# Performance work log

Measured on AMD Instinct MI355X. Metric: run time of the kernel, lower is better.

## Reference

```python
import jax, jax.numpy as jnp
import numpy as np

B, N, D, H, C = 16, 196, 768, 3072, 10

def setup_inputs() -> dict:
    key = jax.random.key(0)
    ks = jax.random.split(key, 8)
    s1 = 1.0 / np.sqrt(D)
    s2 = 1.0 / np.sqrt(H)
    return {
        "x": jax.random.normal(ks[0], (B, N, D), jnp.float32),
        "y": jax.random.randint(ks[1], (B,), 0, C),
        "W1": jax.random.normal(ks[2], (H, D), jnp.float32) * s1,
        "b1": jax.random.normal(ks[3], (H,), jnp.float32) * 0.01,
        "W2": jax.random.normal(ks[4], (D, H), jnp.float32) * s2,
        "b2": jax.random.normal(ks[5], (D,), jnp.float32) * 0.01,
        "mask_fc1": jax.random.uniform(ks[6], (C, H, D), jnp.float32),
        "mask_fc2": jax.random.uniform(ks[7], (C, D, H), jnp.float32),
    }

def reference(x, y, W1, b1, W2, b2, mask_fc1, mask_fc2):
    # per-sample masked weights: [B, out, in]
    Wm1 = W1[None, :, :] * mask_fc1[y]          # [B, H, D]
    h = jnp.einsum('bni,boi->bno', x, Wm1) + b1  # [B, N, H]
    h = jax.nn.gelu(h, approximate=False)        # act (drop1/norm are identity)
    Wm2 = W2[None, :, :] * mask_fc2[y]           # [B, D, H]
    out = jnp.einsum('bni,boi->bno', h, Wm2) + b2  # [B, N, D]
    return out
```

## Files before the change

### kernel.cpp

```cpp
#include <hip/hip_runtime.h>
#include <hip/hip_bf16.h>
#include <math.h>

#define B_ 16
#define N_ 196
#define D_ 768
#define H_ 3072
#define C_ 10
#define MPAD 256

typedef __attribute__((ext_vector_type(8))) short bf16x8;
typedef __attribute__((ext_vector_type(4))) float f32x4;

__device__ __forceinline__ ushort f2bu(float f) {
    union { float f; unsigned u; } c; c.f = f;
    unsigned u = c.u;
    unsigned r = (u + 0x7FFFu + ((u >> 16) & 1u)) >> 16;
    return (ushort)r;
}

__device__ __forceinline__ void gl_lds16(const ushort* g, ushort* l) {
    __builtin_amdgcn_global_load_lds(
        (const __attribute__((address_space(1))) void*)g,
        (__attribute__((address_space(3))) void*)l, 16, 0, 0);
}

__device__ __forceinline__ void build_wm_chunk(
    const float* __restrict__ W, const float* __restrict__ mask,
    const int* __restrict__ y, ushort* __restrict__ outw,
    int c, int chunk)
{
    bool used = false;
    #pragma unroll
    for (int t = 0; t < B_; ++t) used |= (y[t] == c);
    if (!used) return;
    const long n = (long)H_ * D_;
    const long i = (long)chunk * 2048 + threadIdx.x * 8;
    const float4* wp = reinterpret_cast<const float4*>(W + i);
    const float4* mp = reinterpret_cast<const float4*>(mask + c * n + i);
    float4 w0 = wp[0], w1 = wp[1], m0 = mp[0], m1 = mp[1];
    ushort t8[8] = { f2bu(w0.x*m0.x), f2bu(w0.y*m0.y), f2bu(w0.z*m0.z), f2bu(w0.w*m0.w),
                     f2bu(w1.x*m1.x), f2bu(w1.y*m1.y), f2bu(w1.z*m1.z), f2bu(w1.w*m1.w) };
    *reinterpret_cast<uint4*>(outw + c * n + i) = *reinterpret_cast<const uint4*>(t8);
}

template<int EPI>
__device__ __forceinline__ void gemm_core(
    const ushort* __restrict__ A0, const ushort* __restrict__ Wm,
    const int* __restrict__ y, const float* __restrict__ bias1,
    ushort* __restrict__ hout, float* __restrict__ pout,
    int ot, int mt, int b, int sk)
{
    constexpr int K = (EPI == 0) ? D_ : H_;
    __shared__ ushort As[128][64];
    __shared__ ushort Bs[128][64];

    const int cls = y[b];
    const int tid = threadIdx.x, lane = tid & 63, wid = tid >> 6;
    const int wm = wid >> 1, wn = wid & 1;
    const int fr = lane & 15, fq = lane >> 4;
    const int lr = lane >> 3, le = (lane & 7) * 8;

    const ushort* Ab = A0 + ((long)b * MPAD + mt * 128) * K;
    const ushort* Bb = Wm + (long)cls * ((long)H_ * D_) + (long)(ot * 128) * K;

    f32x4 acc[4][4] = {};
    const int kt0 = (EPI == 0) ? 0 : sk * 12;

    #pragma unroll
    for (int t = 0; t < 12; ++t) {
        const int k0 = (kt0 + t) * 64;
        #pragma unroll
        for (int i = 0; i < 4; ++i) {
            const int r = wid * 32 + i * 8;
            gl_lds16(Ab + (long)(r + lr) * K + k0 + le, &As[r][0]);
        }
        #pragma unroll
        for (int i = 0; i < 4; ++i) {
            const int r = wid * 32 + i * 8;
            gl_lds16(Bb + (long)(r + lr) * K + k0 + le, &Bs[r][0]);
        }
        __syncthreads();
        #pragma unroll
        for (int kk = 0; kk < 64; kk += 32) {
            bf16x8 af[4], bf[4];
            #pragma unroll
            for (int i = 0; i < 4; ++i)
                af[i] = *reinterpret_cast<const bf16x8*>(&As[wm*64 + i*16 + fr][kk + fq*8]);
            #pragma unroll
            for (int j = 0; j < 4; ++j)
                bf[j] = *reinterpret_cast<const bf16x8*>(&Bs[wn*64 + j*16 + fr][kk + fq*8]);
            #pragma unroll
            for (int i = 0; i < 4; ++i)
                #pragma unroll
                for (int j = 0; j < 4; ++j)
                    acc[i][j] = __builtin_amdgcn_mfma_f32_16x16x32_bf16(af[i], bf[j], acc[i][j], 0, 0, 0);
        }
        __syncthreads();
    }

    if (EPI == 0) {
        #pragma unroll
        for (int j = 0; j < 4; ++j) {
            const int o = ot*128 + wn*64 + j*16 + fr;
            const float bias = bias1[o];
            #pragma unroll
            for (int i = 0; i < 4; ++i) {
                #pragma unroll
                for (int e = 0; e < 4; ++e) {
                    const int m = mt*128 + wm*64 + i*16 + fq*4 + e;
                    float v = acc[i][j][e] + bias;
                    v = 0.5f * v * (1.0f + erff(v * 0.70710678118654752f));
                    hout[((long)b * MPAD + m) * H_ + o] = f2bu(v);
                }
            }
        }
    } else {
        float* op = pout + (size_t)sk * (size_t)(B_ * N_ * D_);
        #pragma unroll
        for (int j = 0; j < 4; ++j) {
            const int o = ot*128 + wn*64 + j*16 + fr;
            #pragma unroll
            for (int i = 0; i < 4; ++i) {
                #pragma unroll
                for (int e = 0; e < 4; ++e) {
                    const int m = mt*128 + wm*64 + i*16 + fq*4 + e;
                    if (m < N_)
                        op[((long)b * N_ + m) * D_ + o] = acc[i][j][e];
                }
            }
        }
    }
}

__global__ __launch_bounds__(256) void prep1(
    const float* __restrict__ x, const int* __restrict__ y,
    const float* __restrict__ W1, const float* __restrict__ mask1,
    ushort* __restrict__ xb, ushort* __restrict__ wm1)
{
    const int bid = blockIdx.x;
    if (bid < 11520) {
        build_wm_chunk(W1, mask1, y, wm1, bid / 1152, bid % 1152);
    } else {
        const int i = (bid - 11520) * 256 + threadIdx.x;
        const int r = i / 96;
        const int c8 = (i % 96) * 8;
        const int b = r / 196, n = r - b * 196;
        const float4* src = reinterpret_cast<const float4*>(x + (long)r * D_ + c8);
        float4 a = src[0], bb = src[1];
        ushort t[8] = { f2bu(a.x), f2bu(a.y), f2bu(a.z), f2bu(a.w),
                        f2bu(bb.x), f2bu(bb.y), f2bu(bb.z), f2bu(bb.w) };
        *reinterpret_cast<uint4*>(xb + ((long)b * MPAD + n) * D_ + c8) =
            *reinterpret_cast<const uint4*>(t);
    }
}

__global__ __launch_bounds__(256) void fat2(
    const ushort* __restrict__ xb, const ushort* __restrict__ wm1,
    const int* __restrict__ y, const float* __restrict__ b1,
    ushort* __restrict__ h,
    const float* __restrict__ W2, const float* __restrict__ mask2,
    ushort* __restrict__ wm2)
{
    const int bid = blockIdx.x;
    if (bid < 768) {
        const int ot = bid % 24, mt = (bid / 24) & 1, b = bid / 48;
        gemm_core<0>(xb, wm1, y, b1, h, nullptr, ot, mt, b, 0);
    } else {
        const int idx = bid - 768;
        build_wm_chunk(W2, mask2, y, wm2, idx / 1152, idx % 1152);
    }
}

__global__ __launch_bounds__(256) void mgemm2(
    const ushort* __restrict__ h, const ushort* __restrict__ wm2,
    const int* __restrict__ y, float* __restrict__ part)
{
    const int ot = blockIdx.x, mt = blockIdx.y, z = blockIdx.z;
    gemm_core<1>(h, wm2, y, nullptr, nullptr, part, ot, mt, z >> 2, z & 3);
}

__global__ __launch_bounds__(256) void reduce_k(const float* __restrict__ part,
                                                const float* __restrict__ b2,
                                                float* __restrict__ out, int SK)
{
    const int i = blockIdx.x * 256 + threadIdx.x;
    const int stride4 = B_ * N_ * D_ / 4;
    float4 s = reinterpret_cast<const float4*>(part)[i];
    for (int k = 1; k < SK; ++k) {
        float4 p = reinterpret_cast<const float4*>(part)[(size_t)k * stride4 + i];
        s.x += p.x; s.y += p.y; s.z += p.z; s.w += p.w;
    }
    const int ob = (i % (D_ / 4)) * 4;
    float4 bias = *reinterpret_cast<const float4*>(b2 + ob);
    s.x += bias.x; s.y += bias.y; s.z += bias.z; s.w += bias.w;
    reinterpret_cast<float4*>(out)[i] = s;
}

__global__ __launch_bounds__(256) void fb_gemm1(
    const float* __restrict__ x, const int* __restrict__ y,
    const float* __restrict__ W1, const float* __restrict__ b1,
    const float* __restrict__ mask1, ushort* __restrict__ h)
{
    __shared__ ushort As[128][72];
    __shared__ ushort Bs[64][72];
    const int ot = blockIdx.x, mt = blockIdx.y, b = blockIdx.z;
    const int cls = y[b];
    const int tid = threadIdx.x, lane = tid & 63, wid = tid >> 6;
    const int wm = wid >> 1, wn = wid & 1;
    const int fr = lane & 15, fq = lane >> 4;
    const int sr = tid >> 2, sc = (tid & 3) * 16;
    f32x4 acc[4][2] = {};
    const long xbase = ((long)b * N_) * D_;
    const long wbase = (long)(ot * 64) * D_;
    const long mbase = ((long)cls * H_ + ot * 64) * D_;
    for (int kt = 0; kt < D_ / 64; ++kt) {
        const int k0 = kt * 64 + sc;
        #pragma unroll
        for (int half = 0; half < 2; ++half) {
            const int r = sr + half * 64;
            const int m = mt * 128 + r;
            ushort tmp[16];
            if (m < N_) {
                const float4* src = reinterpret_cast<const float4*>(x + xbase + (long)m * D_ + k0);
                #pragma unroll
                for (int j = 0; j < 4; ++j) {
                    float4 v = src[j];
                    tmp[4*j+0]=f2bu(v.x); tmp[4*j+1]=f2bu(v.y); tmp[4*j+2]=f2bu(v.z); tmp[4*j+3]=f2bu(v.w);
                }
            } else { for (int j = 0; j < 16; ++j) tmp[j] = 0; }
            *reinterpret_cast<uint4*>(&As[r][sc])   = *reinterpret_cast<const uint4*>(&tmp[0]);
            *reinterpret_cast<uint4*>(&As[r][sc+8]) = *reinterpret_cast<const uint4*>(&tmp[8]);
        }
        {
            const float4* wsrc = reinterpret_cast<const float4*>(W1 + wbase + (long)sr * D_ + k0);
            const float4* msrc = reinterpret_cast<const float4*>(mask1 + mbase + (long)sr * D_ + k0);
            ushort tmp[16];
            #pragma unroll
            for (int j = 0; j < 4; ++j) {
                float4 wv = wsrc[j], mv = msrc[j];
                tmp[4*j+0]=f2bu(wv.x*mv.x); tmp[4*j+1]=f2bu(wv.y*mv.y);
                tmp[4*j+2]=f2bu(wv.z*mv.z); tmp[4*j+3]=f2bu(wv.w*mv.w);
            }
            *reinterpret_cast<uint4*>(&Bs[sr][sc])   = *reinterpret_cast<const uint4*>(&tmp[0]);
            *reinterpret_cast<uint4*>(&Bs[sr][sc+8]) = *reinterpret_cast<const uint4*>(&tmp[8]);
        }
        __syncthreads();
        #pragma unroll
        for (int kk = 0; kk < 64; kk += 32) {
            bf16x8 af[4], bf[2];
            #pragma unroll
            for (int i = 0; i < 4; ++i) af[i] = *reinterpret_cast<const bf16x8*>(&As[wm*64+i*16+fr][kk+fq*8]);
            #pragma unroll
            for (int j = 0; j < 2; ++j) bf[j] = *reinterpret_cast<const bf16x8*>(&Bs[wn*32+j*16+fr][kk+fq*8]);
            #pragma unroll
            for (int i = 0; i < 4; ++i)
                #pragma unroll
                for (int j = 0; j < 2; ++j)
                    acc[i][j] = __builtin_amdgcn_mfma_f32_16x16x32_bf16(af[i], bf[j], acc[i][j], 0, 0, 0);
        }
        __syncthreads();
    }
    #pragma unroll
    for (int j = 0; j < 2; ++j) {
        const int o = ot*64 + wn*32 + j*16 + fr;
        const float bias = b1[o];
        #pragma unroll
        for (int i = 0; i < 4; ++i)
            #pragma unroll
            for (int e = 0; e < 4; ++e) {
                const int m = mt*128 + wm*64 + i*16 + fq*4 + e;
                if (m < N_) {
                    float v = acc[i][j][e] + bias;
                    v = 0.5f * v * (1.0f + erff(v * 0.70710678118654752f));
                    h[(((long)b * N_) + m) * H_ + o] = f2bu(v);
                }
            }
    }
}

__global__ __launch_bounds__(256) void fb_gemm2(
    const ushort* __restrict__ h, const int* __restrict__ y,
    const float* __restrict__ W2, const float* __restrict__ b2,
    const float* __restrict__ mask2, float* __restrict__ dst,
    int split, int nkt, int add_bias)
{
    __shared__ ushort As[128][72];
    __shared__ ushort Bs[64][72];
    const int ot = blockIdx.x, mt = blockIdx.y, z = blockIdx.z;
    const int b = z / split, sk = z - b * split;
    const int cls = y[b];
    const int tid = threadIdx.x, lane = tid & 63, wid = tid >> 6;
    const int wm = wid >> 1, wn = wid & 1;
    const int fr = lane & 15, fq = lane >> 4;
    const int sr = tid >> 2, sc = (tid & 3) * 16;
    f32x4 acc[4][2] = {};
    const long hbase = ((long)b * N_) * H_;
    const long wbase = (long)(ot * 64) * H_;
    const long mbase = ((long)cls * D_ + ot * 64) * H_;
    const int kt0 = sk * nkt;
    for (int kt = kt0; kt < kt0 + nkt; ++kt) {
        const int k0 = kt * 64 + sc;
        #pragma unroll
        for (int half = 0; half < 2; ++half) {
            const int r = sr + half * 64;
            const int m = mt * 128 + r;
            if (m < N_) {
                const uint4* src = reinterpret_cast<const uint4*>(h + hbase + (long)m * H_ + k0);
                *reinterpret_cast<uint4*>(&As[r][sc])   = src[0];
                *reinterpret_cast<uint4*>(&As[r][sc+8]) = src[1];
            } else {
                uint4 z4 = {0u,0u,0u,0u};
                *reinterpret_cast<uint4*>(&As[r][sc])   = z4;
                *reinterpret_cast<uint4*>(&As[r][sc+8]) = z4;
            }
        }
        {
            const float4* wsrc = reinterpret_cast<const float4*>(W2 + wbase + (long)sr * H_ + k0);
            const float4* msrc = reinterpret_cast<const float4*>(mask2 + mbase + (long)sr * H_ + k0);
            ushort tmp[16];
            #pragma unroll
            for (int j = 0; j < 4; ++j) {
                float4 wv = wsrc[j], mv = msrc[j];
                tmp[4*j+0]=f2bu(wv.x*mv.x); tmp[4*j+1]=f2bu(wv.y*mv.y);
                tmp[4*j+2]=f2bu(wv.z*mv.z); tmp[4*j+3]=f2bu(wv.w*mv.w);
            }
            *reinterpret_cast<uint4*>(&Bs[sr][sc])   = *reinterpret_cast<const uint4*>(&tmp[0]);
            *reinterpret_cast<uint4*>(&Bs[sr][sc+8]) = *reinterpret_cast<const uint4*>(&tmp[8]);
        }
        __syncthreads();
        #pragma unroll
        for (int kk = 0; kk < 64; kk += 32) {
            bf16x8 af[4], bf[2];
            #pragma unroll
            for (int i = 0; i < 4; ++i) af[i] = *reinterpret_cast<const bf16x8*>(&As[wm*64+i*16+fr][kk+fq*8]);
            #pragma unroll
            for (int j = 0; j < 2; ++j) bf[j] = *reinterpret_cast<const bf16x8*>(&Bs[wn*32+j*16+fr][kk+fq*8]);
            #pragma unroll
            for (int i = 0; i < 4; ++i)
                #pragma unroll
                for (int j = 0; j < 2; ++j)
                    acc[i][j] = __builtin_amdgcn_mfma_f32_16x16x32_bf16(af[i], bf[j], acc[i][j], 0, 0, 0);
        }
        __syncthreads();
    }
    float* op = dst + (size_t)sk * (size_t)(B_ * N_ * D_);
    #pragma unroll
    for (int j = 0; j < 2; ++j) {
        const int o = ot*64 + wn*32 + j*16 + fr;
        const float bias = add_bias ? b2[o] : 0.0f;
        #pragma unroll
        for (int i = 0; i < 4; ++i)
            #pragma unroll
            for (int e = 0; e < 4; ++e) {
                const int m = mt*128 + wm*64 + i*16 + fq*4 + e;
                if (m < N_) op[(((long)b * N_) + m) * D_ + o] = acc[i][j][e] + bias;
            }
    }
}

extern "C" void kernel_launch(void* const* d_in, const int* in_sizes, int n_in,
                              void* d_out, int out_size, void* d_ws, size_t ws_size,
                              hipStream_t stream) {
    const float* x  = (const float*)d_in[0];
    const int*   y  = (const int*)d_in[1];
    const float* W1 = (const float*)d_in[2];
    const float* b1 = (const float*)d_in[3];
    const float* W2 = (const float*)d_in[4];
    const float* b2 = (const float*)d_in[5];
    const float* m1 = (const float*)d_in[6];
    const float* m2 = (const float*)d_in[7];
    float* out = (float*)d_out;

    const size_t xbB  = (size_t)B_ * MPAD * D_ * 2;
    const size_t hB   = (size_t)B_ * MPAD * H_ * 2;
    const size_t oB   = (size_t)B_ * N_ * D_ * 4;
    const size_t wmB  = (size_t)C_ * H_ * D_ * 2;

    const size_t off_xb   = 0;
    const size_t off_h    = off_xb + xbB;
    const size_t off_part = off_h + hB;
    const size_t off_wm1  = off_part + 4 * oB;
    const size_t off_wm2  = off_wm1 + wmB;
    const size_t need     = off_wm2 + wmB;

    if (ws_size >= need) {
        ushort* xb  = (ushort*)((char*)d_ws + off_xb);
        ushort* h   = (ushort*)((char*)d_ws + off_h);
        float* part = (float*)((char*)d_ws + off_part);
        ushort* wm1 = (ushort*)((char*)d_ws + off_wm1);
        ushort* wm2 = (ushort*)((char*)d_ws + off_wm2);

        prep1<<<11520 + 1176, 256, 0, stream>>>(x, y, W1, m1, xb, wm1);
        fat2<<<768 + 11520, 256, 0, stream>>>(xb, wm1, y, b1, h, W2, m2, wm2);
        mgemm2<<<dim3(6, 2, 64), 256, 0, stream>>>(h, wm2, y, part);
        reduce_k<<<(B_ * N_ * D_ / 4) / 256, 256, 0, stream>>>(part, b2, out, 4);
    } else {
        const size_t fb_hB = (size_t)B_ * N_ * H_ * 2;
        ushort* h = (ushort*)d_ws;
        int SK = 0;
        if      (ws_size >= fb_hB + 4 * oB) SK = 4;
        else if (ws_size >= fb_hB + 2 * oB) SK = 2;
        float* part = (float*)((char*)d_ws + fb_hB);
        dim3 g1(H_ / 64, 2, B_);
        fb_gemm1<<<g1, 256, 0, stream>>>(x, y, W1, b1, m1, h);
        if (SK) {
            dim3 g2(D_ / 64, 2, B_ * SK);
            fb_gemm2<<<g2, 256, 0, stream>>>(h, y, W2, b2, m2, part, SK, 48 / SK, 0);
            reduce_k<<<(B_ * N_ * D_ / 4) / 256, 256, 0, stream>>>(part, b2, out, SK);
        } else {
            dim3 g2(D_ / 64, 2, B_);
            fb_gemm2<<<g2, 256, 0, stream>>>(h, y, W2, b2, m2, out, 1, 48, 1);
        }
    }
}
```

Before: 142.1 us.

## Merge weight-mask prep into one grid-stride kernel and halve GEMM N-tiles

All masked-weight builds for both layers and the x conversion now run in a single persistent grid-stride prep kernel, and the used-class set is computed once as a bitmask. The layer-2 weight build is no longer co-scheduled with GEMM1. Both GEMMs move from 128x128 to 128x64 output tiles, doubling the block count (1536 blocks each) for better CU fill on the many-CU device. The cost is more A-tile reloads per output and lower MFMA work per LDS load.

```diff
diff --git a/kernel.cpp b/kernel.cpp
--- a/kernel.cpp
+++ b/kernel.cpp
@@ -19,156 +19,130 @@
     return (ushort)r;
 }
 
+__device__ __forceinline__ uint2 pack4(float4 a, float4 b) {
+    ushort t[4] = { f2bu(a.x*b.x), f2bu(a.y*b.y), f2bu(a.z*b.z), f2bu(a.w*b.w) };
+    return *reinterpret_cast<const uint2*>(t);
+}
+
 __device__ __forceinline__ void gl_lds16(const ushort* g, ushort* l) {
     __builtin_amdgcn_global_load_lds(
         (const __attribute__((address_space(1))) void*)g,
         (__attribute__((address_space(3))) void*)l, 16, 0, 0);
 }
 
-__device__ __forceinline__ void build_wm_chunk(
-    const float* __restrict__ W, const float* __restrict__ mask,
-    const int* __restrict__ y, ushort* __restrict__ outw,
-    int c, int chunk)
-{
-    bool used = false;
-    #pragma unroll
-    for (int t = 0; t < B_; ++t) used |= (y[t] == c);
-    if (!used) return;
-    const long n = (long)H_ * D_;
-    const long i = (long)chunk * 2048 + threadIdx.x * 8;
-    const float4* wp = reinterpret_cast<const float4*>(W + i);
-    const float4* mp = reinterpret_cast<const float4*>(mask + c * n + i);
-    float4 w0 = wp[0], w1 = wp[1], m0 = mp[0], m1 = mp[1];
-    ushort t8[8] = { f2bu(w0.x*m0.x), f2bu(w0.y*m0.y), f2bu(w0.z*m0.z), f2bu(w0.w*m0.w),
-                     f2bu(w1.x*m1.x), f2bu(w1.y*m1.y), f2bu(w1.z*m1.z), f2bu(w1.w*m1.w) };
-    *reinterpret_cast<uint4*>(outw + c * n + i) = *reinterpret_cast<const uint4*>(t8);
-}
-
-template<int EPI>
-__device__ __forceinline__ void gemm_core(
-    const ushort* __restrict__ A0, const ushort* __restrict__ Wm,
-    const int* __restrict__ y, const float* __restrict__ bias1,
-    ushort* __restrict__ hout, float* __restrict__ pout,
-    int ot, int mt, int b, int sk)
-{
-    constexpr int K = (EPI == 0) ? D_ : H_;
+__global__ __launch_bounds__(256) void prep_all(
+    const float* __restrict__ x, const int* __restrict__ y,
+    const float* __restrict__ W1, const float* __restrict__ m1,
+    const float* __restrict__ W2, const float* __restrict__ m2,
+    ushort* __restrict__ xb, ushort* __restrict__ wm1, ushort* __restrict__ wm2)
+{
+    unsigned used = 0;
+    #pragma unroll
+    for (int t = 0; t < B_; ++t) used |= (1u << y[t]);
+    const int tid = threadIdx.x;
+
+    for (int u = blockIdx.x; u < 12108; u += gridDim.x) {
+        if (u < 11520) {
+            const int layer = u / 5760;
+            const int v = u - layer * 5760;
+            const int c = v / 576, chunk = v - (v / 576) * 576;
+            if (!((used >> c) & 1)) continue;
+            const float* W = layer ? W2 : W1;
+            const float* M = layer ? m2 : m1;
+            ushort*     O = layer ? wm2 : wm1;
+            const long n = (long)H_ * D_;
+            const float4* wp = reinterpret_cast<const float4*>(W + (long)chunk * 4096);
+            const float4* mp = reinterpret_cast<const float4*>(M + c * n + (long)chunk * 4096);
+            float4 w0 = wp[tid], w1 = wp[tid+256], w2v = wp[tid+512], w3 = wp[tid+768];
+            float4 q0 = mp[tid], q1 = mp[tid+256], q2  = mp[tid+512], q3 = mp[tid+768];
+            uint2* op = reinterpret_cast<uint2*>(O + c * n + (long)chunk * 4096);
+            op[tid]     = pack4(w0, q0);
+            op[tid+256] = pack4(w1, q1);
+            op[tid+512] = pack4(w2v, q2);
+            op[tid+768] = pack4(w3, q3);
+        } else {
+            const int v = u - 11520;
+            const float4* xp = reinterpret_cast<const float4*>(x);
+            const float4 one = {1.f, 1.f, 1.f, 1.f};
+            #pragma unroll
+            for (int k = 0; k < 4; ++k) {
+                const int i4 = v * 1024 + tid + k * 256;
+                const int r  = i4 / 192;
+                const int c4 = i4 - r * 192;
+                const int b = r / N_, nn = r - b * N_;
+                float4 a = xp[i4];
+                *reinterpret_cast<uint2*>(xb + ((long)b * MPAD + nn) * D_ + c4 * 4) =
+                    pack4(a, one);
+            }
+        }
+    }
+}
+
+__global__ __launch_bounds__(256) void mgemm1(
+    const ushort* __restrict__ xb, const ushort* __restrict__ wm1,
+    const int* __restrict__ y, const float* __restrict__ b1,
+    ushort* __restrict__ h)
+{
     __shared__ ushort As[128][64];
-    __shared__ ushort Bs[128][64];
-
+    __shared__ ushort Bs[64][64];
+    const int ot = blockIdx.x;
+    const int mt = blockIdx.y;
+    const int b  = blockIdx.z;
     const int cls = y[b];
     const int tid = threadIdx.x, lane = tid & 63, wid = tid >> 6;
     const int wm = wid >> 1, wn = wid & 1;
     const int fr = lane & 15, fq = lane >> 4;
     const int lr = lane >> 3, le = (lane & 7) * 8;
 
-    const ushort* Ab = A0 + ((long)b * MPAD + mt * 128) * K;
-    const ushort* Bb = Wm + (long)cls * ((long)H_ * D_) + (long)(ot * 128) * K;
-
-    f32x4 acc[4][4] = {};
-    const int kt0 = (EPI == 0) ? 0 : sk * 12;
-
+    const ushort* Ab = xb + ((long)b * MPAD + mt * 128) * D_;
+    const ushort* Bb = wm1 + (long)cls * ((long)H_ * D_) + (long)(ot * 64) * D_;
+
+    f32x4 acc[4][2] = {};
     #pragma unroll
     for (int t = 0; t < 12; ++t) {
-        const int k0 = (kt0 + t) * 64;
+        const int k0 = t * 64;
         #pragma unroll
         for (int i = 0; i < 4; ++i) {
             const int r = wid * 32 + i * 8;
-            gl_lds16(Ab + (long)(r + lr) * K + k0 + le, &As[r][0]);
-        }
+            gl_lds16(Ab + (long)(r + lr) * D_ + k0 + le, &As[r][0]);
+        }
+        #pragma unroll
+        for (int i = 0; i < 2; ++i) {
+            const int r = wid * 16 + i * 8;
+            gl_lds16(Bb + (long)(r + lr) * D_ + k0 + le, &Bs[r][0]);
+        }
+        __syncthreads();
+        #pragma unroll
+        for (int kk = 0; kk < 64; kk += 32) {
+            bf16x8 af[4], bf[2];
+            #pragma unroll
+            for (int i = 0; i < 4; ++i)
+                af[i] = *reinterpret_cast<const bf16x8*>(&As[wm*64 + i*16 + fr][kk + fq*8]);
+            #pragma unroll
+            for (int j = 0; j < 2; ++j)
+                bf[j] = *reinterpret_cast<const bf16x8*>(&Bs[wn*32 + j*16 + fr][kk + fq*8]);
+            #pragma unroll
+            for (int i = 0; i < 4; ++i)
+                #pragma unroll
+                for (int j = 0; j < 2; ++j)
+                    acc[i][j] = __builtin_amdgcn_mfma_f32_16x16x32_bf16(af[i], bf[j], acc[i][j], 0, 0, 0);
+        }
+        __syncthreads();
+    }
+    #pragma unroll
+    for (int j = 0; j < 2; ++j) {
+        const int o = ot*64 + wn*32 + j*16 + fr;
+        const float bias = b1[o];
         #pragma unroll
         for (int i = 0; i < 4; ++i) {
-            const int r = wid * 32 + i * 8;
-            gl_lds16(Bb + (long)(r + lr) * K + k0 + le, &Bs[r][0]);
-        }
-        __syncthreads();
-        #pragma unroll
-        for (int kk = 0; kk < 64; kk += 32) {
-            bf16x8 af[4], bf[4];
-            #pragma unroll
-            for (int i = 0; i < 4; ++i)
-                af[i] = *reinterpret_cast<const bf16x8*>(&As[wm*64 + i*16 + fr][kk + fq*8]);
-            #pragma unroll
-            for (int j = 0; j < 4; ++j)
-                bf[j] = *reinterpret_cast<const bf16x8*>(&Bs[wn*64 + j*16 + fr][kk + fq*8]);
-            #pragma unroll
-            for (int i = 0; i < 4; ++i)
-                #pragma unroll
-                for (int j = 0; j < 4; ++j)
-                    acc[i][j] = __builtin_amdgcn_mfma_f32_16x16x32_bf16(af[i], bf[j], acc[i][j], 0, 0, 0);
-        }
-        __syncthreads();
-    }
-
-    if (EPI == 0) {
-        #pragma unroll
-        for (int j = 0; j < 4; ++j) {
-            const int o = ot*128 + wn*64 + j*16 + fr;
-            const float bias = bias1[o];
-            #pragma unroll
-            for (int i = 0; i < 4; ++i) {
-                #pragma unroll
-                for (int e = 0; e < 4; ++e) {
-                    const int m = mt*128 + wm*64 + i*16 + fq*4 + e;
-                    float v = acc[i][j][e] + bias;
-                    v = 0.5f * v * (1.0f + erff(v * 0.70710678118654752f));
-                    hout[((long)b * MPAD + m) * H_ + o] = f2bu(v);
-                }
-            }
-        }
-    } else {
-        float* op = pout + (size_t)sk * (size_t)(B_ * N_ * D_);
-        #pragma unroll
-        for (int j = 0; j < 4; ++j) {
-            const int o = ot*128 + wn*64 + j*16 + fr;
-            #pragma unroll
-            for (int i = 0; i < 4; ++i) {
-                #pragma unroll
-                for (int e = 0; e < 4; ++e) {
-                    const int m = mt*128 + wm*64 + i*16 + fq*4 + e;
-                    if (m < N_)
-                        op[((long)b * N_ + m) * D_ + o] = acc[i][j][e];
-                }
-            }
-        }
-    }
-}
-
-__global__ __launch_bounds__(256) void prep1(
-    const float* __restrict__ x, const int* __restrict__ y,
-    const float* __restrict__ W1, const float* __restrict__ mask1,
-    ushort* __restrict__ xb, ushort* __restrict__ wm1)
-{
-    const int bid = blockIdx.x;
-    if (bid < 11520) {
-        build_wm_chunk(W1, mask1, y, wm1, bid / 1152, bid % 1152);
-    } else {
-        const int i = (bid - 11520) * 256 + threadIdx.x;
-        const int r = i / 96;
-        const int c8 = (i % 96) * 8;
-        const int b = r / 196, n = r - b * 196;
-        const float4* src = reinterpret_cast<const float4*>(x + (long)r * D_ + c8);
-        float4 a = src[0], bb = src[1];
-        ushort t[8] = { f2bu(a.x), f2bu(a.y), f2bu(a.z), f2bu(a.w),
-                        f2bu(bb.x), f2bu(bb.y), f2bu(bb.z), f2bu(bb.w) };
-        *reinterpret_cast<uint4*>(xb + ((long)b * MPAD + n) * D_ + c8) =
-            *reinterpret_cast<const uint4*>(t);
-    }
-}
-
-__global__ __launch_bounds__(256) void fat2(
-    const ushort* __restrict__ xb, const ushort* __restrict__ wm1,
-    const int* __restrict__ y, const float* __restrict__ b1,
-    ushort* __restrict__ h,
-    const float* __restrict__ W2, const float* __restrict__ mask2,
-    ushort* __restrict__ wm2)
-{
-    const int bid = blockIdx.x;
-    if (bid < 768) {
-        const int ot = bid % 24, mt = (bid / 24) & 1, b = bid / 48;
-        gemm_core<0>(xb, wm1, y, b1, h, nullptr, ot, mt, b, 0);
-    } else {
-        const int idx = bid - 768;
-        build_wm_chunk(W2, mask2, y, wm2, idx / 1152, idx % 1152);
+            #pragma unroll
+            for (int e = 0; e < 4; ++e) {
+                const int m = mt*128 + wm*64 + i*16 + fq*4 + e;
+                float v = acc[i][j][e] + bias;
+                v = 0.5f * v * (1.0f + erff(v * 0.70710678118654752f));
+                h[((long)b * MPAD + m) * H_ + o] = f2bu(v);
+            }
+        }
     }
 }
 
@@ -176,8 +150,68 @@
     const ushort* __restrict__ h, const ushort* __restrict__ wm2,
     const int* __restrict__ y, float* __restrict__ part)
 {
-    const int ot = blockIdx.x, mt = blockIdx.y, z = blockIdx.z;
-    gemm_core<1>(h, wm2, y, nullptr, nullptr, part, ot, mt, z >> 2, z & 3);
+    __shared__ ushort As[128][64];
+    __shared__ ushort Bs[64][64];
+    const int ot = blockIdx.x;
+    const int mt = blockIdx.y;
+    const int z  = blockIdx.z;
+    const int b = z >> 2, sk = z & 3;
+    const int cls = y[b];
+    const int tid = threadIdx.x, lane = tid & 63, wid = tid >> 6;
+    const int wm = wid >> 1, wn = wid & 1;
+    const int fr = lane & 15, fq = lane >> 4;
+    const int lr = lane >> 3, le = (lane & 7) * 8;
+
+    const ushort* Ab = h + ((long)b * MPAD + mt * 128) * H_;
+    const ushort* Bb = wm2 + (long)cls * ((long)H_ * D_) + (long)(ot * 64) * H_;
+
+    f32x4 acc[4][2] = {};
+    const int kt0 = sk * 12;
+    #pragma unroll
+    for (int t = 0; t < 12; ++t) {
+        const int k0 = (kt0 + t) * 64;
+        #pragma unroll
+        for (int i = 0; i < 4; ++i) {
+            const int r = wid * 32 + i * 8;
+            gl_lds16(Ab + (long)(r + lr) * H_ + k0 + le, &As[r][0]);
+        }
+        #pragma unroll
+        for (int i = 0; i < 2; ++i) {
+            const int r = wid * 16 + i * 8;
+            gl_lds16(Bb + (long)(r + lr) * H_ + k0 + le, &Bs[r][0]);
+        }
+        __syncthreads();
+        #pragma unroll
+        for (int kk = 0; kk < 64; kk += 32) {
+            bf16x8 af[4], bf[2];
+            #pragma unroll
+            for (int i = 0; i < 4; ++i)
+                af[i] = *reinterpret_cast<const bf16x8*>(&As[wm*64 + i*16 + fr][kk + fq*8]);
+            #pragma unroll
+            for (int j = 0; j < 2; ++j)
+                bf[j] = *reinterpret_cast<const bf16x8*>(&Bs[wn*32 + j*16 + fr][kk + fq*8]);
+            #pragma unroll
+            for (int i = 0; i < 4; ++i)
+                #pragma unroll
+                for (int j = 0; j < 2; ++j)
+                    acc[i][j] = __builtin_amdgcn_mfma_f32_16x16x32_bf16(af[i], bf[j], acc[i][j], 0, 0, 0);
+        }
+        __syncthreads();
+    }
+    float* op = part + (size_t)sk * (size_t)(B_ * N_ * D_);
+    #pragma unroll
+    for (int j = 0; j < 2; ++j) {
+        const int o = ot*64 + wn*32 + j*16 + fr;
+        #pragma unroll
+        for (int i = 0; i < 4; ++i) {
+            #pragma unroll
+            for (int e = 0; e < 4; ++e) {
+                const int m = mt*128 + wm*64 + i*16 + fq*4 + e;
+                if (m < N_)
+                    op[((long)b * N_ + m) * D_ + o] = acc[i][j][e];
+            }
+        }
+    }
 }
 
 __global__ __launch_bounds__(256) void reduce_k(const float* __restrict__ part,
@@ -391,9 +425,9 @@
         ushort* wm1 = (ushort*)((char*)d_ws + off_wm1);
         ushort* wm2 = (ushort*)((char*)d_ws + off_wm2);
 
-        prep1<<<11520 + 1176, 256, 0, stream>>>(x, y, W1, m1, xb, wm1);
-        fat2<<<768 + 11520, 256, 0, stream>>>(xb, wm1, y, b1, h, W2, m2, wm2);
-        mgemm2<<<dim3(6, 2, 64), 256, 0, stream>>>(h, wm2, y, part);
+        prep_all<<<2048, 256, 0, stream>>>(x, y, W1, m1, W2, m2, xb, wm1, wm2);
+        mgemm1<<<dim3(48, 2, 16), 256, 0, stream>>>(xb, wm1, y, b1, h);
+        mgemm2<<<dim3(12, 2, 64), 256, 0, stream>>>(h, wm2, y, part);
         reduce_k<<<(B_ * N_ * D_ / 4) / 256, 256, 0, stream>>>(part, b2, out, 4);
     } else {
         const size_t fb_hB = (size_t)B_ * N_ * H_ * 2;
```

Result: slower. 161.6 us (+13.8%).

## Double-buffer GEMM LDS tiles, halve N-tile, and merge weight prep into one kernel

Applied to the files above, without the earlier changes.

Both masked-weight builds (fc1 and fc2) and the x conversion now run in a single prep kernel. This removes the fused GEMM1-plus-W2-prep kernel, and GEMM1 becomes a plain launch. The GEMM core now double-buffers the A and B tiles in LDS, issuing the next tile's global-to-LDS loads before the current tile's MFMAs, so memory latency overlaps compute. It also shrinks the output tile from 128 to 64 columns, which doubles the grid and improves occupancy and CU coverage. The trade-offs are more A-tile reloads per output and the loss of the earlier overlap between GEMM1 and W2 preparation.

```diff
diff --git a/kernel.cpp b/kernel.cpp
--- a/kernel.cpp
+++ b/kernel.cpp
@@ -25,23 +25,45 @@
         (__attribute__((address_space(3))) void*)l, 16, 0, 0);
 }
 
-__device__ __forceinline__ void build_wm_chunk(
-    const float* __restrict__ W, const float* __restrict__ mask,
-    const int* __restrict__ y, ushort* __restrict__ outw,
-    int c, int chunk)
-{
-    bool used = false;
-    #pragma unroll
-    for (int t = 0; t < B_; ++t) used |= (y[t] == c);
-    if (!used) return;
-    const long n = (long)H_ * D_;
-    const long i = (long)chunk * 2048 + threadIdx.x * 8;
-    const float4* wp = reinterpret_cast<const float4*>(W + i);
-    const float4* mp = reinterpret_cast<const float4*>(mask + c * n + i);
-    float4 w0 = wp[0], w1 = wp[1], m0 = mp[0], m1 = mp[1];
-    ushort t8[8] = { f2bu(w0.x*m0.x), f2bu(w0.y*m0.y), f2bu(w0.z*m0.z), f2bu(w0.w*m0.w),
-                     f2bu(w1.x*m1.x), f2bu(w1.y*m1.y), f2bu(w1.z*m1.z), f2bu(w1.w*m1.w) };
-    *reinterpret_cast<uint4*>(outw + c * n + i) = *reinterpret_cast<const uint4*>(t8);
+__global__ __launch_bounds__(256) void prep_all(
+    const float* __restrict__ x, const int* __restrict__ y,
+    const float* __restrict__ W1, const float* __restrict__ m1,
+    const float* __restrict__ W2, const float* __restrict__ m2,
+    ushort* __restrict__ xb, ushort* __restrict__ wm1, ushort* __restrict__ wm2)
+{
+    const int bid = blockIdx.x;
+    const int tid = threadIdx.x;
+    if (bid < 23040) {
+        const int layer = bid / 11520;
+        const int v = bid - layer * 11520;
+        const int c = v / 1152, chunk = v - c * 1152;
+        bool used = false;
+        #pragma unroll
+        for (int t = 0; t < B_; ++t) used |= (y[t] == c);
+        if (!used) return;
+        const float* W = layer ? W2 : W1;
+        const float* M = layer ? m2 : m1;
+        ushort*      O = layer ? wm2 : wm1;
+        const long n = (long)H_ * D_;
+        const long i = (long)chunk * 2048 + tid * 8;
+        const float4* wp = reinterpret_cast<const float4*>(W + i);
+        const float4* mp = reinterpret_cast<const float4*>(M + c * n + i);
+        float4 w0 = wp[0], w1 = wp[1], q0 = mp[0], q1 = mp[1];
+        ushort t8[8] = { f2bu(w0.x*q0.x), f2bu(w0.y*q0.y), f2bu(w0.z*q0.z), f2bu(w0.w*q0.w),
+                         f2bu(w1.x*q1.x), f2bu(w1.y*q1.y), f2bu(w1.z*q1.z), f2bu(w1.w*q1.w) };
+        *reinterpret_cast<uint4*>(O + c * n + i) = *reinterpret_cast<const uint4*>(t8);
+    } else {
+        const int i = (bid - 23040) * 256 + tid;
+        const int r = i / 96;
+        const int c8 = (i % 96) * 8;
+        const int b = r / N_, nn = r - b * N_;
+        const float4* src = reinterpret_cast<const float4*>(x + (long)r * D_ + c8);
+        float4 a = src[0], bb = src[1];
+        ushort t8[8] = { f2bu(a.x), f2bu(a.y), f2bu(a.z), f2bu(a.w),
+                         f2bu(bb.x), f2bu(bb.y), f2bu(bb.z), f2bu(bb.w) };
+        *reinterpret_cast<uint4*>(xb + ((long)b * MPAD + nn) * D_ + c8) =
+            *reinterpret_cast<const uint4*>(t8);
+    }
 }
 
 template<int EPI>
@@ -52,8 +74,9 @@
     int ot, int mt, int b, int sk)
 {
     constexpr int K = (EPI == 0) ? D_ : H_;
-    __shared__ ushort As[128][64];
-    __shared__ ushort Bs[128][64];
+    constexpr int NT = 12;
+    __shared__ ushort As[2][128][64];
+    __shared__ ushort Bs[2][64][64];
 
     const int cls = y[b];
     const int tid = threadIdx.x, lane = tid & 63, wid = tid >> 6;
@@ -62,47 +85,67 @@
     const int lr = lane >> 3, le = (lane & 7) * 8;
 
     const ushort* Ab = A0 + ((long)b * MPAD + mt * 128) * K;
-    const ushort* Bb = Wm + (long)cls * ((long)H_ * D_) + (long)(ot * 128) * K;
-
-    f32x4 acc[4][4] = {};
-    const int kt0 = (EPI == 0) ? 0 : sk * 12;
-
-    #pragma unroll
-    for (int t = 0; t < 12; ++t) {
-        const int k0 = (kt0 + t) * 64;
+    const ushort* Bb = Wm + (long)cls * ((long)H_ * D_) + (long)(ot * 64) * K;
+    const int kt0 = (EPI == 0) ? 0 : sk * NT;
+
+    {
+        const int k0 = kt0 * 64;
         #pragma unroll
         for (int i = 0; i < 4; ++i) {
             const int r = wid * 32 + i * 8;
-            gl_lds16(Ab + (long)(r + lr) * K + k0 + le, &As[r][0]);
-        }
-        #pragma unroll
-        for (int i = 0; i < 4; ++i) {
-            const int r = wid * 32 + i * 8;
-            gl_lds16(Bb + (long)(r + lr) * K + k0 + le, &Bs[r][0]);
-        }
-        __syncthreads();
+            gl_lds16(Ab + (long)(r + lr) * K + k0 + le, &As[0][r][0]);
+        }
+        #pragma unroll
+        for (int i = 0; i < 2; ++i) {
+            const int r = wid * 16 + i * 8;
+            gl_lds16(Bb + (long)(r + lr) * K + k0 + le, &Bs[0][r][0]);
+        }
+    }
+    asm volatile("s_waitcnt vmcnt(0)" ::: "memory");
+    __builtin_amdgcn_sched_barrier(0);
+    __builtin_amdgcn_s_barrier();
+
+    f32x4 acc[4][2] = {};
+    #pragma unroll
+    for (int t = 0; t < NT; ++t) {
+        const int cur = t & 1;
+        if (t + 1 < NT) {
+            const int k0 = (kt0 + t + 1) * 64;
+            #pragma unroll
+            for (int i = 0; i < 4; ++i) {
+                const int r = wid * 32 + i * 8;
+                gl_lds16(Ab + (long)(r + lr) * K + k0 + le, &As[cur ^ 1][r][0]);
+            }
+            #pragma unroll
+            for (int i = 0; i < 2; ++i) {
+                const int r = wid * 16 + i * 8;
+                gl_lds16(Bb + (long)(r + lr) * K + k0 + le, &Bs[cur ^ 1][r][0]);
+            }
+        }
         #pragma unroll
         for (int kk = 0; kk < 64; kk += 32) {
-            bf16x8 af[4], bf[4];
+            bf16x8 af[4], bf[2];
             #pragma unroll
             for (int i = 0; i < 4; ++i)
-                af[i] = *reinterpret_cast<const bf16x8*>(&As[wm*64 + i*16 + fr][kk + fq*8]);
-            #pragma unroll
-            for (int j = 0; j < 4; ++j)
-                bf[j] = *reinterpret_cast<const bf16x8*>(&Bs[wn*64 + j*16 + fr][kk + fq*8]);
+                af[i] = *reinterpret_cast<const bf16x8*>(&As[cur][wm*64 + i*16 + fr][kk + fq*8]);
+            #pragma unroll
+            for (int j = 0; j < 2; ++j)
+                bf[j] = *reinterpret_cast<const bf16x8*>(&Bs[cur][wn*32 + j*16 + fr][kk + fq*8]);
             #pragma unroll
             for (int i = 0; i < 4; ++i)
                 #pragma unroll
-                for (int j = 0; j < 4; ++j)
+                for (int j = 0; j < 2; ++j)
                     acc[i][j] = __builtin_amdgcn_mfma_f32_16x16x32_bf16(af[i], bf[j], acc[i][j], 0, 0, 0);
         }
-        __syncthreads();
+        asm volatile("s_waitcnt vmcnt(0)" ::: "memory");
+        __builtin_amdgcn_sched_barrier(0);
+        __builtin_amdgcn_s_barrier();
     }
 
     if (EPI == 0) {
         #pragma unroll
-        for (int j = 0; j < 4; ++j) {
-            const int o = ot*128 + wn*64 + j*16 + fr;
+        for (int j = 0; j < 2; ++j) {
+            const int o = ot*64 + wn*32 + j*16 + fr;
             const float bias = bias1[o];
             #pragma unroll
             for (int i = 0; i < 4; ++i) {
@@ -118,8 +161,8 @@
     } else {
         float* op = pout + (size_t)sk * (size_t)(B_ * N_ * D_);
         #pragma unroll
-        for (int j = 0; j < 4; ++j) {
-            const int o = ot*128 + wn*64 + j*16 + fr;
+        for (int j = 0; j < 2; ++j) {
+            const int o = ot*64 + wn*32 + j*16 + fr;
             #pragma unroll
             for (int i = 0; i < 4; ++i) {
                 #pragma unroll
@@ -133,51 +176,20 @@
     }
 }
 
-__global__ __launch_bounds__(256) void prep1(
-    const float* __restrict__ x, const int* __restrict__ y,
-    const float* __restrict__ W1, const float* __restrict__ mask1,
-    ushort* __restrict__ xb, ushort* __restrict__ wm1)
-{
-    const int bid = blockIdx.x;
-    if (bid < 11520) {
-        build_wm_chunk(W1, mask1, y, wm1, bid / 1152, bid % 1152);
-    } else {
-        const int i = (bid - 11520) * 256 + threadIdx.x;
-        const int r = i / 96;
-        const int c8 = (i % 96) * 8;
-        const int b = r / 196, n = r - b * 196;
-        const float4* src = reinterpret_cast<const float4*>(x + (long)r * D_ + c8);
-        float4 a = src[0], bb = src[1];
-        ushort t[8] = { f2bu(a.x), f2bu(a.y), f2bu(a.z), f2bu(a.w),
-                        f2bu(bb.x), f2bu(bb.y), f2bu(bb.z), f2bu(bb.w) };
-        *reinterpret_cast<uint4*>(xb + ((long)b * MPAD + n) * D_ + c8) =
-            *reinterpret_cast<const uint4*>(t);
-    }
-}
-
-__global__ __launch_bounds__(256) void fat2(
+__global__ __launch_bounds__(256) void mgemm1(
     const ushort* __restrict__ xb, const ushort* __restrict__ wm1,
     const int* __restrict__ y, const float* __restrict__ b1,
-    ushort* __restrict__ h,
-    const float* __restrict__ W2, const float* __restrict__ mask2,
-    ushort* __restrict__ wm2)
-{
-    const int bid = blockIdx.x;
-    if (bid < 768) {
-        const int ot = bid % 24, mt = (bid / 24) & 1, b = bid / 48;
-        gemm_core<0>(xb, wm1, y, b1, h, nullptr, ot, mt, b, 0);
-    } else {
-        const int idx = bid - 768;
-        build_wm_chunk(W2, mask2, y, wm2, idx / 1152, idx % 1152);
-    }
+    ushort* __restrict__ h)
+{
+    gemm_core<0>(xb, wm1, y, b1, h, nullptr, blockIdx.x, blockIdx.y, blockIdx.z, 0);
 }
 
 __global__ __launch_bounds__(256) void mgemm2(
     const ushort* __restrict__ h, const ushort* __restrict__ wm2,
     const int* __restrict__ y, float* __restrict__ part)
 {
-    const int ot = blockIdx.x, mt = blockIdx.y, z = blockIdx.z;
-    gemm_core<1>(h, wm2, y, nullptr, nullptr, part, ot, mt, z >> 2, z & 3);
+    const int z = blockIdx.z;
+    gemm_core<1>(h, wm2, y, nullptr, nullptr, part, blockIdx.x, blockIdx.y, z >> 2, z & 3);
 }
 
 __global__ __launch_bounds__(256) void reduce_k(const float* __restrict__ part,
@@ -391,9 +403,9 @@
         ushort* wm1 = (ushort*)((char*)d_ws + off_wm1);
         ushort* wm2 = (ushort*)((char*)d_ws + off_wm2);
 
-        prep1<<<11520 + 1176, 256, 0, stream>>>(x, y, W1, m1, xb, wm1);
-        fat2<<<768 + 11520, 256, 0, stream>>>(xb, wm1, y, b1, h, W2, m2, wm2);
-        mgemm2<<<dim3(6, 2, 64), 256, 0, stream>>>(h, wm2, y, part);
+        prep_all<<<23040 + 1176, 256, 0, stream>>>(x, y, W1, m1, W2, m2, xb, wm1, wm2);
+        mgemm1<<<dim3(48, 2, 16), 256, 0, stream>>>(xb, wm1, y, b1, h);
+        mgemm2<<<dim3(12, 2, 64), 256, 0, stream>>>(h, wm2, y, part);
         reduce_k<<<(B_ * N_ * D_ / 4) / 256, 256, 0, stream>>>(part, b2, out, 4);
     } else {
         const size_t fb_hB = (size_t)B_ * N_ * H_ * 2;
```

New measurement: 174.8 us. +23.0%, slower.

## Fuse mask multiply and bf16 conversion into GEMM B-tile loads

Applied to the files above, without the earlier changes.

Drops the separate passes that built bf16 masked weight tensors for every used class. Each GEMM block now reads the fp32 weight and the per-class mask for its tile, multiplies them, converts to bf16 and writes the result into padded shared memory. This removes the masked-weight write and re-read traffic, two large prep launches and their workspace. In exchange, fp32 weights and masks are read repeatedly across blocks, and the B tile now goes through registers with synchronous loads instead of async global-to-LDS loads, which may expose more memory latency.

```diff
diff --git a/kernel.cpp b/kernel.cpp
--- a/kernel.cpp
+++ b/kernel.cpp
@@ -25,35 +25,33 @@
         (__attribute__((address_space(3))) void*)l, 16, 0, 0);
 }
 
-__device__ __forceinline__ void build_wm_chunk(
-    const float* __restrict__ W, const float* __restrict__ mask,
-    const int* __restrict__ y, ushort* __restrict__ outw,
-    int c, int chunk)
-{
-    bool used = false;
-    #pragma unroll
-    for (int t = 0; t < B_; ++t) used |= (y[t] == c);
-    if (!used) return;
-    const long n = (long)H_ * D_;
-    const long i = (long)chunk * 2048 + threadIdx.x * 8;
-    const float4* wp = reinterpret_cast<const float4*>(W + i);
-    const float4* mp = reinterpret_cast<const float4*>(mask + c * n + i);
-    float4 w0 = wp[0], w1 = wp[1], m0 = mp[0], m1 = mp[1];
-    ushort t8[8] = { f2bu(w0.x*m0.x), f2bu(w0.y*m0.y), f2bu(w0.z*m0.z), f2bu(w0.w*m0.w),
-                     f2bu(w1.x*m1.x), f2bu(w1.y*m1.y), f2bu(w1.z*m1.z), f2bu(w1.w*m1.w) };
-    *reinterpret_cast<uint4*>(outw + c * n + i) = *reinterpret_cast<const uint4*>(t8);
+__global__ __launch_bounds__(256) void cvt_x(const float* __restrict__ x,
+                                             ushort* __restrict__ xb) {
+    const int i = blockIdx.x * 256 + threadIdx.x;
+    const int r = i / 96;
+    const int c8 = (i % 96) * 8;
+    const int b = r / N_, nn = r - b * N_;
+    const float4* src = reinterpret_cast<const float4*>(x + (long)r * D_ + c8);
+    float4 a = src[0], bb = src[1];
+    ushort t8[8] = { f2bu(a.x), f2bu(a.y), f2bu(a.z), f2bu(a.w),
+                     f2bu(bb.x), f2bu(bb.y), f2bu(bb.z), f2bu(bb.w) };
+    *reinterpret_cast<uint4*>(xb + ((long)b * MPAD + nn) * D_ + c8) =
+        *reinterpret_cast<const uint4*>(t8);
 }
 
 template<int EPI>
 __device__ __forceinline__ void gemm_core(
-    const ushort* __restrict__ A0, const ushort* __restrict__ Wm,
-    const int* __restrict__ y, const float* __restrict__ bias1,
+    const ushort* __restrict__ A0, const float* __restrict__ W,
+    const float* __restrict__ M, const int* __restrict__ y,
+    const float* __restrict__ bias1,
     ushort* __restrict__ hout, float* __restrict__ pout,
     int ot, int mt, int b, int sk)
 {
     constexpr int K = (EPI == 0) ? D_ : H_;
+    constexpr int OH = (EPI == 0) ? H_ : D_;
+    constexpr int NT = 12;
     __shared__ ushort As[128][64];
-    __shared__ ushort Bs[128][64];
+    __shared__ ushort Bs[128][72];
 
     const int cls = y[b];
     const int tid = threadIdx.x, lane = tid & 63, wid = tid >> 6;
@@ -62,13 +60,17 @@
     const int lr = lane >> 3, le = (lane & 7) * 8;
 
     const ushort* Ab = A0 + ((long)b * MPAD + mt * 128) * K;
-    const ushort* Bb = Wm + (long)cls * ((long)H_ * D_) + (long)(ot * 128) * K;
+    const float*  Wb = W + (long)(ot * 128) * K;
+    const float*  Mb = M + ((long)cls * OH + ot * 128) * K;
+
+    const int sr0 = tid >> 2;
+    const int scb = (tid & 3) * 16;
 
     f32x4 acc[4][4] = {};
-    const int kt0 = (EPI == 0) ? 0 : sk * 12;
+    const int kt0 = (EPI == 0) ? 0 : sk * NT;
 
     #pragma unroll
-    for (int t = 0; t < 12; ++t) {
+    for (int t = 0; t < NT; ++t) {
         const int k0 = (kt0 + t) * 64;
         #pragma unroll
         for (int i = 0; i < 4; ++i) {
@@ -76,9 +78,18 @@
             gl_lds16(Ab + (long)(r + lr) * K + k0 + le, &As[r][0]);
         }
         #pragma unroll
-        for (int i = 0; i < 4; ++i) {
-            const int r = wid * 32 + i * 8;
-            gl_lds16(Bb + (long)(r + lr) * K + k0 + le, &Bs[r][0]);
+        for (int p = 0; p < 2; ++p) {
+            const int r = p * 64 + sr0;
+            const float4* wp = reinterpret_cast<const float4*>(Wb + (long)r * K + k0 + scb);
+            const float4* mp = reinterpret_cast<const float4*>(Mb + (long)r * K + k0 + scb);
+            float4 w0 = wp[0], w1 = wp[1], w2v = wp[2], w3 = wp[3];
+            float4 q0 = mp[0], q1 = mp[1], q2  = mp[2], q3 = mp[3];
+            ushort ta[8] = { f2bu(w0.x*q0.x), f2bu(w0.y*q0.y), f2bu(w0.z*q0.z), f2bu(w0.w*q0.w),
+                             f2bu(w1.x*q1.x), f2bu(w1.y*q1.y), f2bu(w1.z*q1.z), f2bu(w1.w*q1.w) };
+            ushort tb[8] = { f2bu(w2v.x*q2.x), f2bu(w2v.y*q2.y), f2bu(w2v.z*q2.z), f2bu(w2v.w*q2.w),
+                             f2bu(w3.x*q3.x), f2bu(w3.y*q3.y), f2bu(w3.z*q3.z), f2bu(w3.w*q3.w) };
+            *reinterpret_cast<uint4*>(&Bs[r][scb])     = *reinterpret_cast<const uint4*>(ta);
+            *reinterpret_cast<uint4*>(&Bs[r][scb + 8]) = *reinterpret_cast<const uint4*>(tb);
         }
         __syncthreads();
         #pragma unroll
@@ -133,51 +144,21 @@
     }
 }
 
-__global__ __launch_bounds__(256) void prep1(
-    const float* __restrict__ x, const int* __restrict__ y,
-    const float* __restrict__ W1, const float* __restrict__ mask1,
-    ushort* __restrict__ xb, ushort* __restrict__ wm1)
-{
-    const int bid = blockIdx.x;
-    if (bid < 11520) {
-        build_wm_chunk(W1, mask1, y, wm1, bid / 1152, bid % 1152);
-    } else {
-        const int i = (bid - 11520) * 256 + threadIdx.x;
-        const int r = i / 96;
-        const int c8 = (i % 96) * 8;
-        const int b = r / 196, n = r - b * 196;
-        const float4* src = reinterpret_cast<const float4*>(x + (long)r * D_ + c8);
-        float4 a = src[0], bb = src[1];
-        ushort t[8] = { f2bu(a.x), f2bu(a.y), f2bu(a.z), f2bu(a.w),
-                        f2bu(bb.x), f2bu(bb.y), f2bu(bb.z), f2bu(bb.w) };
-        *reinterpret_cast<uint4*>(xb + ((long)b * MPAD + n) * D_ + c8) =
-            *reinterpret_cast<const uint4*>(t);
-    }
-}
-
-__global__ __launch_bounds__(256) void fat2(
-    const ushort* __restrict__ xb, const ushort* __restrict__ wm1,
-    const int* __restrict__ y, const float* __restrict__ b1,
-    ushort* __restrict__ h,
-    const float* __restrict__ W2, const float* __restrict__ mask2,
-    ushort* __restrict__ wm2)
-{
-    const int bid = blockIdx.x;
-    if (bid < 768) {
-        const int ot = bid % 24, mt = (bid / 24) & 1, b = bid / 48;
-        gemm_core<0>(xb, wm1, y, b1, h, nullptr, ot, mt, b, 0);
-    } else {
-        const int idx = bid - 768;
-        build_wm_chunk(W2, mask2, y, wm2, idx / 1152, idx % 1152);
-    }
-}
-
-__global__ __launch_bounds__(256) void mgemm2(
-    const ushort* __restrict__ h, const ushort* __restrict__ wm2,
-    const int* __restrict__ y, float* __restrict__ part)
-{
-    const int ot = blockIdx.x, mt = blockIdx.y, z = blockIdx.z;
-    gemm_core<1>(h, wm2, y, nullptr, nullptr, part, ot, mt, z >> 2, z & 3);
+__global__ __launch_bounds__(256) void fg1(
+    const ushort* __restrict__ xb, const float* __restrict__ W1,
+    const float* __restrict__ m1, const int* __restrict__ y,
+    const float* __restrict__ b1, ushort* __restrict__ h)
+{
+    gemm_core<0>(xb, W1, m1, y, b1, h, nullptr, blockIdx.x, blockIdx.y, blockIdx.z, 0);
+}
+
+__global__ __launch_bounds__(256) void fg2(
+    const ushort* __restrict__ h, const float* __restrict__ W2,
+    const float* __restrict__ m2, const int* __restrict__ y,
+    float* __restrict__ part)
+{
+    const int z = blockIdx.z;
+    gemm_core<1>(h, W2, m2, y, nullptr, nullptr, part, blockIdx.x, blockIdx.y, z >> 2, z & 3);
 }
 
 __global__ __launch_bounds__(256) void reduce_k(const float* __restrict__ part,
@@ -375,25 +356,20 @@
     const size_t xbB  = (size_t)B_ * MPAD * D_ * 2;
     const size_t hB   = (size_t)B_ * MPAD * H_ * 2;
     const size_t oB   = (size_t)B_ * N_ * D_ * 4;
-    const size_t wmB  = (size_t)C_ * H_ * D_ * 2;
 
     const size_t off_xb   = 0;
     const size_t off_h    = off_xb + xbB;
     const size_t off_part = off_h + hB;
-    const size_t off_wm1  = off_part + 4 * oB;
-    const size_t off_wm2  = off_wm1 + wmB;
-    const size_t need     = off_wm2 + wmB;
+    const size_t need     = off_part + 4 * oB;
 
     if (ws_size >= need) {
         ushort* xb  = (ushort*)((char*)d_ws + off_xb);
         ushort* h   = (ushort*)((char*)d_ws + off_h);
         float* part = (float*)((char*)d_ws + off_part);
-        ushort* wm1 = (ushort*)((char*)d_ws + off_wm1);
-        ushort* wm2 = (ushort*)((char*)d_ws + off_wm2);
-
-        prep1<<<11520 + 1176, 256, 0, stream>>>(x, y, W1, m1, xb, wm1);
-        fat2<<<768 + 11520, 256, 0, stream>>>(xb, wm1, y, b1, h, W2, m2, wm2);
-        mgemm2<<<dim3(6, 2, 64), 256, 0, stream>>>(h, wm2, y, part);
+
+        cvt_x<<<1176, 256, 0, stream>>>(x, xb);
+        fg1<<<dim3(24, 2, 16), 256, 0, stream>>>(xb, W1, m1, y, b1, h);
+        fg2<<<dim3(6, 2, 64), 256, 0, stream>>>(h, W2, m2, y, part);
         reduce_k<<<(B_ * N_ * D_ / 4) / 256, 256, 0, stream>>>(part, b2, out, 4);
     } else {
         const size_t fb_hB = (size_t)B_ * N_ * H_ * 2;
```

Result: slower. 152.0 us (+7.0%).
